# Optimization experiments

Hardware: AMD Instinct MI355X
Metric: run time of the kernel (lower is better)

Reference implementation:

```python
import jax, jax.numpy as jnp
import numpy as np

INPUTS = 512    # feature dim per timestep == seq len T == max_length (required by module math)
HIDDEN = 512
OUTPUTS = 512
MAXLEN = INPUTS
BATCH = 256


def setup_inputs() -> dict:
    key = jax.random.key(0)
    ks = jax.random.split(key, 7)
    def lin(k, out_f, in_f):
        bound = 1.0 / np.sqrt(in_f)
        return jax.random.uniform(k, (out_f, in_f), jnp.float32, -bound, bound)
    return {
        "x": jax.random.normal(ks[0], (BATCH, INPUTS * MAXLEN), jnp.float32),
        "W_attn": lin(ks[1], MAXLEN, HIDDEN + INPUTS),
        "b_attn": jnp.zeros((MAXLEN,), jnp.float32),
        "W_comb": lin(ks[2], HIDDEN, INPUTS + MAXLEN),
        "b_comb": jnp.zeros((HIDDEN,), jnp.float32),
        "W_ih": lin(ks[3], 3 * HIDDEN, HIDDEN),
        "W_hh": lin(ks[4], 3 * HIDDEN, HIDDEN),
        "b_ih": jnp.zeros((3 * HIDDEN,), jnp.float32),
        "b_hh": jnp.zeros((3 * HIDDEN,), jnp.float32),
        "W_out": lin(ks[5], OUTPUTS, HIDDEN),
        "b_out": jnp.zeros((OUTPUTS,), jnp.float32),
    }


def reference(x, W_attn, b_attn, W_comb, b_comb, W_ih, W_hh, b_ih, b_hh, W_out, b_out):
    B = x.shape[0]
    H = HIDDEN
    xv = x.reshape(B, INPUTS, MAXLEN)      # [B, inputs, T]
    xs = jnp.transpose(xv, (2, 0, 1))      # [T, B, inputs] for scan over time

    def step(h, x_t):
        # Bahdanau-style attention over the inputs axis (M == inputs)
        aw = jax.nn.softmax(jnp.concatenate([x_t, h], axis=1) @ W_attn.T + b_attn, axis=1)  # [B, M]
        ctx = jnp.einsum('bm,bmt->bt', aw, xv)                                              # [B, T]
        g = jax.nn.relu(jnp.concatenate([x_t, ctx], axis=1) @ W_comb.T + b_comb)            # [B, H]
        # PyTorch GRU cell, gate order (r, z, n)
        gi = g @ W_ih.T + b_ih
        gh = h @ W_hh.T + b_hh
        r = jax.nn.sigmoid(gi[:, :H] + gh[:, :H])
        z = jax.nn.sigmoid(gi[:, H:2 * H] + gh[:, H:2 * H])
        n = jnp.tanh(gi[:, 2 * H:] + r * gh[:, 2 * H:])
        h_new = (1.0 - z) * n + z * h
        return h_new, None

    h0 = jnp.zeros((B, H), x.dtype)
    hT, _ = jax.lax.scan(step, h0, xs)
    return hT @ W_out.T + b_out  # [B, outputs]
```

## Files before the change

kernel.cpp:

```cpp
#include <hip/hip_runtime.h>

#define NB 256
#define NT 512
#define NI 512
#define NH 512
#define NG 1536
#define NBLK 512

typedef __attribute__((ext_vector_type(8))) short bf16x8;
typedef __attribute__((ext_vector_type(4))) float f32x4;
typedef __attribute__((ext_vector_type(2))) float f32x2;

#define MFMA(a, b, c) __builtin_amdgcn_mfma_f32_16x16x32_bf16((a), (b), (c), 0, 0, 0)

#define BAR_LEAF(g)   ((g) * 64)
#define BAR_ROOT      1024
#define BAR_GEN       1088
#define FLG_LOGIT(rt) (1152 + (rt) * 64)
#define FLG_GH(rt)    (1664 + (rt) * 64)
#define FLG_XT        1920
#define FLG_G(rg)     (2176 + (rg) * 64)
#define FLG_GP(b)     (2688 + (b) * 64)
#define BAR_WORDS     20480

__device__ __forceinline__ unsigned short f2bf(float f) {
  unsigned int u = __float_as_uint(f);
  u = u + 0x7FFFu + ((u >> 16) & 1u);
  return (unsigned short)(u >> 16);
}
__device__ __forceinline__ float bflo(unsigned int p) { return __uint_as_float(p << 16); }
__device__ __forceinline__ float bfhi(unsigned int p) { return __uint_as_float(p & 0xffff0000u); }
__device__ __forceinline__ float sigm(float x) { return 1.f / (1.f + __expf(-x)); }

__device__ __forceinline__ void stf(float* p, float v) {
  __hip_atomic_store(p, v, __ATOMIC_RELAXED, __HIP_MEMORY_SCOPE_AGENT);
}
__device__ __forceinline__ void stu32(void* p, unsigned v) {
  __hip_atomic_store((unsigned*)p, v, __ATOMIC_RELAXED, __HIP_MEMORY_SCOPE_AGENT);
}
__device__ __forceinline__ void stu64(void* p, unsigned long long v) {
  __hip_atomic_store((unsigned long long*)p, v, __ATOMIC_RELAXED, __HIP_MEMORY_SCOPE_AGENT);
}
__device__ __forceinline__ void ldg16(uint4& d, const void* p) {
  asm volatile("global_load_dwordx4 %0, %1, off sc1" : "=v"(d) : "v"(p));
}
__device__ __forceinline__ void ldg8(float2& d, const void* p) {
  asm volatile("global_load_dwordx2 %0, %1, off sc1" : "=v"(d) : "v"(p));
}
__device__ __forceinline__ void ldg4(float& d, const void* p) {
  asm volatile("global_load_dword %0, %1, off sc1" : "=v"(d) : "v"(p));
}
__device__ __forceinline__ void wait_vm0() {
  asm volatile("s_waitcnt vmcnt(0)" ::: "memory");
  __builtin_amdgcn_sched_barrier(0);
}
__device__ __forceinline__ bf16x8 as_frag(uint4 v) {
  union { uint4 u; bf16x8 f; } c; c.u = v; return c.f;
}

__device__ __forceinline__ void flag_add(unsigned* f) {
  __hip_atomic_fetch_add(f, 1u, __ATOMIC_RELAXED, __HIP_MEMORY_SCOPE_AGENT);
}
__device__ __forceinline__ void flag_wait(unsigned* f, unsigned target) {
  while (__hip_atomic_load(f, __ATOMIC_RELAXED, __HIP_MEMORY_SCOPE_AGENT) < target)
    __builtin_amdgcn_s_sleep(1);
}

__global__ __launch_bounds__(256) void cast_f32_bf16(const float* __restrict__ s,
                                                     unsigned short* __restrict__ d, int n) {
  int i = blockIdx.x * 256 + threadIdx.x;
  int stride = gridDim.x * 256;
  for (; i < n; i += stride) d[i] = f2bf(s[i]);
}

__global__ __launch_bounds__(256) void zt_fp8(unsigned short* __restrict__ XZ,
                                              float* __restrict__ Zsc,
                                              const unsigned short* __restrict__ Wc) {
  __shared__ unsigned short As[32][552];
  __shared__ float Zf[32][512];
  const int tid = threadIdx.x;
  const int row0 = blockIdx.x * 32;
  const uint4* src = (const uint4*)(XZ + (size_t)row0 * 512);
#pragma unroll
  for (int it = 0; it < 8; ++it) {
    int e8 = tid + it * 256;
    uint4 v = src[e8];
    *(uint4*)&As[e8 >> 6][(e8 & 63) * 8] = v;
  }
  __syncthreads();
  const int lane = tid & 63, w = tid >> 6;
  const int al = lane & 15, kg = lane >> 4;
  const int rbase = (w & 1) * 16;
  const int cbase = (w >> 1) * 256;
  for (int cc = 0; cc < 16; ++cc) {
    int col0 = cbase + cc * 16;
    f32x4 acc = {0.f, 0.f, 0.f, 0.f};
    const unsigned short* Bp = Wc + (size_t)(col0 + al) * 1024 + 512;
    for (int k = 0; k < 512; k += 32) {
      bf16x8 av = *(const bf16x8*)&As[rbase + al][k + kg * 8];
      bf16x8 bv = *(const bf16x8*)(Bp + k + kg * 8);
      acc = MFMA(av, bv, acc);
    }
#pragma unroll
    for (int r = 0; r < 4; ++r)
      Zf[rbase + kg * 4 + r][col0 + al] = acc[r];
  }
  __syncthreads();
  unsigned char* Z8 = (unsigned char*)XZ;
#pragma unroll 2
  for (int r8 = 0; r8 < 8; ++r8) {
    int row = w * 8 + r8;
    const float* vr = &Zf[row][lane * 8];
    float v0 = vr[0], v1 = vr[1], v2 = vr[2], v3 = vr[3];
    float v4 = vr[4], v5 = vr[5], v6 = vr[6], v7 = vr[7];
    float amax = fmaxf(fmaxf(fmaxf(fabsf(v0), fabsf(v1)), fmaxf(fabsf(v2), fabsf(v3))),
                       fmaxf(fmaxf(fabsf(v4), fabsf(v5)), fmaxf(fabsf(v6), fabsf(v7))));
#pragma unroll
    for (int off = 32; off >= 1; off >>= 1) amax = fmaxf(amax, __shfl_xor(amax, off));
    float inv = amax > 0.f ? 448.f / amax : 0.f;
    int w0 = __builtin_amdgcn_cvt_pk_fp8_f32(v0 * inv, v1 * inv, 0, false);
    w0 = __builtin_amdgcn_cvt_pk_fp8_f32(v2 * inv, v3 * inv, w0, true);
    int w1 = __builtin_amdgcn_cvt_pk_fp8_f32(v4 * inv, v5 * inv, 0, false);
    w1 = __builtin_amdgcn_cvt_pk_fp8_f32(v6 * inv, v7 * inv, w1, true);
    uint2 o; o.x = (unsigned)w0; o.y = (unsigned)w1;
    *(uint2*)(Z8 + ((size_t)(row0 + row) << 10) + lane * 8) = o;
    if (lane == 0) Zsc[row0 + row] = amax * (1.f / 448.f);
  }
}

__global__ __launch_bounds__(256) void init_kernel(const float* __restrict__ x,
                                                   unsigned short* __restrict__ Xt,
                                                   unsigned short* __restrict__ Hbf,
                                                   unsigned* __restrict__ bar) {
  int idx = blockIdx.x * 256 + threadIdx.x;
  if (idx < BAR_WORDS) bar[idx] = 0u;
  if (idx < NB * NI) {
    int b = idx >> 9, i = idx & 511;
    Xt[idx] = f2bf(x[((size_t)b * 512 + i) * 512]);
    Hbf[idx] = 0;
  }
}

__global__ __launch_bounds__(256) void lxgx0_kernel(const unsigned short* __restrict__ Xt0,
                                                    const unsigned short* __restrict__ Wa,
                                                    const unsigned short* __restrict__ Wc,
                                                    const float* __restrict__ b_comb,
                                                    float* __restrict__ Lx,
                                                    float* __restrict__ Gx) {
  const int tid = threadIdx.x, lane = tid & 63, w = tid >> 6;
  const int al = lane & 15, kg = lane >> 4;
  int T = blockIdx.x;
  int m = T >> 7, tt = T & 127;
  int rt = tt >> 4, ct = tt & 15;
  int row0 = rt * 32 + (w & 1) * 16, col0 = ct * 32 + (w >> 1) * 16;
  const unsigned short* A = Xt0 + (size_t)(row0 + al) * NI;
  const unsigned short* B = (m ? Wc : Wa) + (size_t)(col0 + al) * 1024;
  f32x4 acc = {0.f, 0.f, 0.f, 0.f};
  for (int k = 0; k < 512; k += 32)
    acc = MFMA(*(const bf16x8*)(A + k + kg * 8), *(const bf16x8*)(B + k + kg * 8), acc);
  float* dst = m ? Gx : Lx;
  float bias = m ? b_comb[col0 + al] : 0.f;
#pragma unroll
  for (int r = 0; r < 4; ++r) {
    int row = row0 + kg * 4 + r;
    dst[row * NI + col0 + al] = acc[r] + bias;
  }
}

struct KParams {
  const unsigned char* Z8;
  const float* Zsc;
  const unsigned short* Wa;
  const unsigned short* Whh;
  const unsigned short* Wc;
  const unsigned short* Wih;
  const unsigned short* Wout;
  unsigned short* Xt;
  unsigned short* Hbf;
  unsigned short* Gbf;
  float* logits;
  float* gh;
  float* Lx;
  float* Gx;
  float* Gp;
  const float* x;
  const float* b_attn;
  const float* b_hh;
  const float* b_ih;
  const float* b_comb;
  const float* b_out;
  float* out;
  unsigned* bar;
};

__device__ __forceinline__ void gbar(unsigned* bar, unsigned gen_expect) {
  asm volatile("s_waitcnt vmcnt(0)" ::: "memory");
  __syncthreads();
  if (threadIdx.x == 0) {
    unsigned old = __hip_atomic_fetch_add(&bar[BAR_LEAF(blockIdx.x >> 5)], 1u,
                                          __ATOMIC_RELAXED, __HIP_MEMORY_SCOPE_AGENT);
    if ((old & 31) == 31) {
      unsigned ro = __hip_atomic_fetch_add(&bar[BAR_ROOT], 1u,
                                           __ATOMIC_RELAXED, __HIP_MEMORY_SCOPE_AGENT);
      if ((ro & 15) == 15)
        __hip_atomic_fetch_add(&bar[BAR_GEN], 1u,
                               __ATOMIC_RELAXED, __HIP_MEMORY_SCOPE_AGENT);
    }
    while (__hip_atomic_load(&bar[BAR_GEN], __ATOMIC_RELAXED, __HIP_MEMORY_SCOPE_AGENT) < gen_expect)
      __builtin_amdgcn_s_sleep(2);
    asm volatile("" ::: "memory");
  }
  __syncthreads();
}

__global__ __launch_bounds__(256, 2) void persistent_kernel(KParams P) {
  __shared__ float aw[512];
  __shared__ float4 pA[4][64];
  __shared__ float4 pB[4][64];
  __shared__ float red[8];
  const int bid = blockIdx.x, tid = threadIdx.x;
  const int lane = tid & 63, w = tid >> 6;
  const int al = lane & 15, kg = lane >> 4;

  f32x4 hreg = {0.f, 0.f, 0.f, 0.f};

  for (int t = 0; t < NT; ++t) {
    const int p = t & 1, np = p ^ 1;
    if (bid < 128) {
      int rt = bid >> 4, ct = bid & 15;
      int row0 = rt * 32 + (w & 1) * 16, col0 = ct * 32 + (w >> 1) * 16;
      const unsigned short* Ah = P.Hbf + (size_t)(row0 + al) * NH;
      const unsigned short* B = P.Wa + (size_t)(col0 + al) * 1024 + 512;
      uint4 fh[16];
      float lx[4];
#pragma unroll
      for (int i = 0; i < 16; ++i) ldg16(fh[i], Ah + i * 32 + kg * 8);
      {
        const float* lxp = P.Lx + (size_t)p * (NB * NI) + (size_t)(row0 + kg * 4) * NI + col0 + al;
#pragma unroll
        for (int r = 0; r < 4; ++r) ldg4(lx[r], lxp + (size_t)r * NI);
      }
      wait_vm0();
      f32x4 a1 = {0.f, 0.f, 0.f, 0.f};
#pragma unroll
      for (int i = 0; i < 16; ++i)
        a1 = MFMA(as_frag(fh[i]), *(const bf16x8*)(B + i * 32 + kg * 8), a1);
#pragma unroll
      for (int r = 0; r < 4; ++r) {
        int row = row0 + kg * 4 + r;
        stf(&P.logits[row * NI + col0 + al], lx[r] + a1[r] + P.b_attn[col0 + al]);
      }
      __syncthreads();
      if (tid == 0) flag_add(&P.bar[FLG_LOGIT(rt)]);
    } else if (bid < 320) {
      int bb = bid - 128;
      int rt = bb / 48, ct = bb % 48;
      int row0 = rt * 64 + w * 16, col0 = ct * 32;
      const unsigned short* Ah = P.Hbf + (size_t)(row0 + al) * NH;
      const unsigned short* B0 = P.Whh + (size_t)(col0 + al) * 512;
      const unsigned short* B1 = P.Whh + (size_t)(col0 + 16 + al) * 512;
      uint4 fa[16];
#pragma unroll
      for (int i = 0; i < 16; ++i) ldg16(fa[i], Ah + i * 32 + kg * 8);
      wait_vm0();
      f32x4 a0 = {0.f, 0.f, 0.f, 0.f}, a1 = {0.f, 0.f, 0.f, 0.f};
#pragma unroll
      for (int i = 0; i < 16; ++i) {
        a0 = MFMA(as_frag(fa[i]), *(const bf16x8*)(B0 + i * 32 + kg * 8), a0);
        a1 = MFMA(as_frag(fa[i]), *(const bf16x8*)(B1 + i * 32 + kg * 8), a1);
      }
#pragma unroll
      for (int r = 0; r < 4; ++r) {
        int row = row0 + kg * 4 + r;
        stf(&P.gh[row * NG + col0 + al], a0[r] + P.b_hh[col0 + al]);
        stf(&P.gh[row * NG + col0 + 16 + al], a1[r] + P.b_hh[col0 + 16 + al]);
      }
      __syncthreads();
      if (tid == 0) flag_add(&P.bar[FLG_GH(rt)]);
    } else if (bid < 384) {
    } else {
      if (t < NT - 1) {
        for (int e2 = (bid - 384) * 256 + tid; e2 < NB * NI / 2; e2 += 128 * 256) {
          int b = e2 >> 8, i = (e2 & 255) * 2;
          const float* xp = P.x + ((size_t)b * 512 + i) * 512 + t + 1;
          unsigned lo = f2bf(xp[0]);
          unsigned hi = f2bf(xp[512]);
          stu32(&P.Xt[(size_t)np * (NB * NI) + b * 512 + i], lo | (hi << 16));
        }
        __syncthreads();
        if (tid == 0) flag_add(&P.bar[FLG_XT]);
      }
    }

    {
      const int b = bid >> 1, mh = bid & 1;
      if (tid == 0) flag_wait(&P.bar[FLG_LOGIT(b >> 5)], 16u * (t + 1));
      __syncthreads();
      float2 lv;
      ldg8(lv, P.logits + (size_t)b * NI + 2 * tid);
      wait_vm0();
      float mx = fmaxf(lv.x, lv.y);
#pragma unroll
      for (int off = 32; off >= 1; off >>= 1) mx = fmaxf(mx, __shfl_xor(mx, off));
      if (lane == 0) red[w] = mx;
      __syncthreads();
      mx = fmaxf(fmaxf(red[0], red[1]), fmaxf(red[2], red[3]));
      float e0 = __expf(lv.x - mx), e1 = __expf(lv.y - mx);
      float sm = e0 + e1;
#pragma unroll
      for (int off = 32; off >= 1; off >>= 1) sm += __shfl_xor(sm, off);
      if (lane == 0) red[4 + w] = sm;
      __syncthreads();
      sm = (red[4] + red[5]) + (red[6] + red[7]);
      float inv = 1.f / sm;
      float2 scl = *(const float2*)(P.Zsc + (size_t)b * 512 + 2 * tid);
      aw[2 * tid] = e0 * inv * scl.x;
      aw[2 * tid + 1] = e1 * inv * scl.y;
      __syncthreads();

      const unsigned char* Zb = P.Z8 + (((size_t)b * 512 + mh * 256 + w * 64) << 10) + lane * 8;
      const float* awp = aw + mh * 256 + w * 64;
      float c0 = 0.f, c1 = 0.f, c2 = 0.f, c3 = 0.f, c4 = 0.f, c5 = 0.f, c6 = 0.f, c7 = 0.f;
#pragma unroll
      for (int mm = 0; mm < 64; mm += 16) {
        uint2 px[16];
#pragma unroll
        for (int u = 0; u < 16; ++u) px[u] = *(const uint2*)(Zb + ((size_t)(mm + u) << 10));
#pragma unroll
        for (int u = 0; u < 16; ++u) {
          float a_ = awp[mm + u];
          f32x2 d0 = __builtin_amdgcn_cvt_pk_f32_fp8((int)px[u].x, false);
          f32x2 d1 = __builtin_amdgcn_cvt_pk_f32_fp8((int)px[u].x, true);
          f32x2 d2 = __builtin_amdgcn_cvt_pk_f32_fp8((int)px[u].y, false);
          f32x2 d3 = __builtin_amdgcn_cvt_pk_f32_fp8((int)px[u].y, true);
          c0 = fmaf(a_, d0[0], c0); c1 = fmaf(a_, d0[1], c1);
          c2 = fmaf(a_, d1[0], c2); c3 = fmaf(a_, d1[1], c3);
          c4 = fmaf(a_, d2[0], c4); c5 = fmaf(a_, d2[1], c5);
          c6 = fmaf(a_, d3[0], c6); c7 = fmaf(a_, d3[1], c7);
        }
      }
      pA[w][lane] = make_float4(c0, c1, c2, c3);
      pB[w][lane] = make_float4(c4, c5, c6, c7);
      __syncthreads();
      float s0_, s1_, s2_, s3_, s4_, s5_, s6_, s7_;
      if (w == 0) {
        float4 a0_ = pA[0][lane], a1_ = pA[1][lane], a2_ = pA[2][lane], a3_ = pA[3][lane];
        float4 b0_ = pB[0][lane], b1_ = pB[1][lane], b2_ = pB[2][lane], b3_ = pB[3][lane];
        s0_ = (a0_.x + a1_.x) + (a2_.x + a3_.x);
        s1_ = (a0_.y + a1_.y) + (a2_.y + a3_.y);
        s2_ = (a0_.z + a1_.z) + (a2_.z + a3_.z);
        s3_ = (a0_.w + a1_.w) + (a2_.w + a3_.w);
        s4_ = (b0_.x + b1_.x) + (b2_.x + b3_.x);
        s5_ = (b0_.y + b1_.y) + (b2_.y + b3_.y);
        s6_ = (b0_.z + b1_.z) + (b2_.z + b3_.z);
        s7_ = (b0_.w + b1_.w) + (b2_.w + b3_.w);
      }
      if (mh == 0) {
        if (w == 0) {
          float* gp = P.Gp + (size_t)b * NH + lane * 8;
          union { float f[2]; unsigned long long q; } q0, q1, q2, q3;
          q0.f[0] = s0_; q0.f[1] = s1_;
          q1.f[0] = s2_; q1.f[1] = s3_;
          q2.f[0] = s4_; q2.f[1] = s5_;
          q3.f[0] = s6_; q3.f[1] = s7_;
          stu64(gp, q0.q); stu64(gp + 2, q1.q); stu64(gp + 4, q2.q); stu64(gp + 6, q3.q);
        }
        __syncthreads();
        if (tid == 0) flag_add(&P.bar[FLG_GP(b)]);
      } else {
        __syncthreads();
        if (tid == 0) flag_wait(&P.bar[FLG_GP(b)], (unsigned)(t + 1));
        __syncthreads();
        if (w == 0) {
          const float* gp = P.Gp + (size_t)b * NH + lane * 8;
          const float* gxp = P.Gx + (size_t)p * (NB * NH) + (size_t)b * NH + lane * 8;
          float2 r0, r1, r2, r3, x0, x1, x2, x3;
          ldg8(r0, gp);     ldg8(r1, gp + 2);
          ldg8(r2, gp + 4); ldg8(r3, gp + 6);
          ldg8(x0, gxp);     ldg8(x1, gxp + 2);
          ldg8(x2, gxp + 4); ldg8(x3, gxp + 6);
          wait_vm0();
          float v0 = fmaxf(x0.x + r0.x + s0_, 0.f);
          float v1 = fmaxf(x0.y + r0.y + s1_, 0.f);
          float v2 = fmaxf(x1.x + r1.x + s2_, 0.f);
          float v3 = fmaxf(x1.y + r1.y + s3_, 0.f);
          float v4 = fmaxf(x2.x + r2.x + s4_, 0.f);
          float v5 = fmaxf(x2.y + r2.y + s5_, 0.f);
          float v6 = fmaxf(x3.x + r3.x + s6_, 0.f);
          float v7 = fmaxf(x3.y + r3.y + s7_, 0.f);
          unsigned long long o0 =
              (unsigned long long)((unsigned)f2bf(v0) | ((unsigned)f2bf(v1) << 16)) |
              ((unsigned long long)((unsigned)f2bf(v2) | ((unsigned)f2bf(v3) << 16)) << 32);
          unsigned long long o1 =
              (unsigned long long)((unsigned)f2bf(v4) | ((unsigned)f2bf(v5) << 16)) |
              ((unsigned long long)((unsigned)f2bf(v6) | ((unsigned)f2bf(v7) << 16)) << 32);
          stu64(P.Gbf + (size_t)b * NH + lane * 8, o0);
          stu64(P.Gbf + (size_t)b * NH + lane * 8 + 4, o1);
        }
        __syncthreads();
        if (tid == 0) flag_add(&P.bar[FLG_G(b >> 5)]);
      }
    }

    if (bid >= 384) {
      int q = bid - 384;
      int rt = q >> 4, ct = q & 15;
      int row0 = rt * 32 + (w & 1) * 16;
      int j0 = ct * 32 + (w >> 1) * 16;
      if (tid == 0) {
        flag_wait(&P.bar[FLG_G(rt)], 32u * (t + 1));
        flag_wait(&P.bar[FLG_GH(rt >> 1)], 48u * (t + 1));
      }
      __syncthreads();
      const unsigned short* Ag = P.Gbf + (size_t)(row0 + al) * NH;
      const unsigned short* Br = P.Wih + (size_t)(j0 + al) * 512;
      const unsigned short* Bz = P.Wih + (size_t)(j0 + 512 + al) * 512;
      const unsigned short* Bn = P.Wih + (size_t)(j0 + 1024 + al) * 512;
      int j = j0 + al;
      uint4 fa[16];
      float ghv[4][3];
#pragma unroll
      for (int i = 0; i < 16; ++i) ldg16(fa[i], Ag + i * 32 + kg * 8);
#pragma unroll
      for (int r = 0; r < 4; ++r) {
        const float* ghrow = P.gh + (size_t)(row0 + kg * 4 + r) * NG + j;
        ldg4(ghv[r][0], ghrow);
        ldg4(ghv[r][1], ghrow + 512);
        ldg4(ghv[r][2], ghrow + 1024);
      }
      wait_vm0();
      f32x4 ar = {0.f, 0.f, 0.f, 0.f}, az = {0.f, 0.f, 0.f, 0.f}, an = {0.f, 0.f, 0.f, 0.f};
#pragma unroll
      for (int i = 0; i < 16; ++i) {
        ar = MFMA(as_frag(fa[i]), *(const bf16x8*)(Br + i * 32 + kg * 8), ar);
        az = MFMA(as_frag(fa[i]), *(const bf16x8*)(Bz + i * 32 + kg * 8), az);
        an = MFMA(as_frag(fa[i]), *(const bf16x8*)(Bn + i * 32 + kg * 8), an);
      }
      float bir = P.b_ih[j], biz = P.b_ih[j + 512], bin_ = P.b_ih[j + 1024];
#pragma unroll
      for (int r = 0; r < 4; ++r) {
        int row = row0 + kg * 4 + r;
        float rg = sigm(ar[r] + bir + ghv[r][0]);
        float zg = sigm(az[r] + biz + ghv[r][1]);
        float ng = tanhf(an[r] + bin_ + rg * ghv[r][2]);
        float hn = (1.f - zg) * ng + zg * hreg[r];
        hreg[r] = hn;
        unsigned hv = f2bf(hn);
        unsigned ov = __shfl_xor((int)hv, 1);
        if ((al & 1) == 0)
          stu32(&P.Hbf[(size_t)row * NH + (j & ~1)], hv | (ov << 16));
      }
    } else if (bid >= 320) {
      if (t < NT - 1) {
        if (tid == 0) flag_wait(&P.bar[FLG_XT], 128u * (t + 1));
        __syncthreads();
        int q = bid - 320;
        for (int jj = 0; jj < 4; ++jj) {
          int T = q + 64 * jj;
          int m = T >> 7, tt = T & 127;
          int rt = tt >> 4, ct = tt & 15;
          int row0 = rt * 32 + (w & 1) * 16, col0 = ct * 32 + (w >> 1) * 16;
          const unsigned short* A = P.Xt + (size_t)np * (NB * NI) + (size_t)(row0 + al) * NI;
          const unsigned short* B = (m ? P.Wc : P.Wa) + (size_t)(col0 + al) * 1024;
          uint4 fa[16];
#pragma unroll
          for (int i = 0; i < 16; ++i) ldg16(fa[i], A + i * 32 + kg * 8);
          wait_vm0();
          f32x4 acc = {0.f, 0.f, 0.f, 0.f};
#pragma unroll
          for (int i = 0; i < 16; ++i)
            acc = MFMA(as_frag(fa[i]), *(const bf16x8*)(B + i * 32 + kg * 8), acc);
          float* dst = (m ? P.Gx : P.Lx) + (size_t)np * (NB * NI);
          float bias = m ? P.b_comb[col0 + al] : 0.f;
#pragma unroll
          for (int r = 0; r < 4; ++r) {
            int row = row0 + kg * 4 + r;
            stf(&dst[row * NI + col0 + al], acc[r] + bias);
          }
        }
      }
    }
    gbar(P.bar, (unsigned)(t + 1));
  }

  if (bid < 128) {
    int rt = bid >> 4, ct = bid & 15;
    int row0 = rt * 32 + (w & 1) * 16;
    int col0 = ct * 32 + (w >> 1) * 16;
    const unsigned short* Ah = P.Hbf + (size_t)(row0 + al) * NH;
    const unsigned short* B0 = P.Wout + (size_t)(col0 + al) * 512;
    uint4 fa[16];
#pragma unroll
    for (int i = 0; i < 16; ++i) ldg16(fa[i], Ah + i * 32 + kg * 8);
    wait_vm0();
    f32x4 acc = {0.f, 0.f, 0.f, 0.f};
#pragma unroll
    for (int i = 0; i < 16; ++i) acc = MFMA(as_frag(fa[i]), *(const bf16x8*)(B0 + i * 32 + kg * 8), acc);
#pragma unroll
    for (int r = 0; r < 4; ++r) {
      int row = row0 + kg * 4 + r;
      P.out[row * 512 + col0 + al] = acc[r] + P.b_out[col0 + al];
    }
  }
}

extern "C" void kernel_launch(void* const* d_in, const int* in_sizes, int n_in,
                              void* d_out, int out_size, void* d_ws, size_t ws_size,
                              hipStream_t stream) {
  const float* x      = (const float*)d_in[0];
  const float* W_attn = (const float*)d_in[1];
  const float* b_attn = (const float*)d_in[2];
  const float* W_comb = (const float*)d_in[3];
  const float* b_comb = (const float*)d_in[4];
  const float* W_ih   = (const float*)d_in[5];
  const float* W_hh   = (const float*)d_in[6];
  const float* b_ih   = (const float*)d_in[7];
  const float* b_hh   = (const float*)d_in[8];
  const float* W_out  = (const float*)d_in[9];
  const float* b_out  = (const float*)d_in[10];

  char* wp = (char*)d_ws;
  size_t off = 0;
  unsigned short* XZ   = (unsigned short*)(wp + off); off += (size_t)NB * NI * NH * 2;
  unsigned short* Wa   = (unsigned short*)(wp + off); off += (size_t)NI * 1024 * 2;
  unsigned short* Whh  = (unsigned short*)(wp + off); off += (size_t)NG * 512 * 2;
  unsigned short* Wc   = (unsigned short*)(wp + off); off += (size_t)NH * 1024 * 2;
  unsigned short* Wih  = (unsigned short*)(wp + off); off += (size_t)NG * 512 * 2;
  unsigned short* Wout = (unsigned short*)(wp + off); off += (size_t)512 * 512 * 2;
  unsigned short* Xt   = (unsigned short*)(wp + off); off += (size_t)2 * NB * NI * 2;
  unsigned short* Hbf  = (unsigned short*)(wp + off); off += (size_t)NB * NH * 2;
  unsigned short* Gbf  = (unsigned short*)(wp + off); off += (size_t)NB * NH * 2;
  float* logits        = (float*)(wp + off); off += (size_t)NB * NI * 4;
  float* gh            = (float*)(wp + off); off += (size_t)NB * NG * 4;
  float* Lx            = (float*)(wp + off); off += (size_t)2 * NB * NI * 4;
  float* Gx            = (float*)(wp + off); off += (size_t)2 * NB * NI * 4;
  float* Gp            = (float*)(wp + off); off += (size_t)NB * NH * 4;
  float* Zsc           = (float*)(wp + off); off += (size_t)NB * NI * 4;
  unsigned* bar        = (unsigned*)(wp + off); off += (size_t)BAR_WORDS * 4 + 4096;

  cast_f32_bf16<<<8192, 256, 0, stream>>>(x, XZ, NB * NI * NT);
  cast_f32_bf16<<<512, 256, 0, stream>>>(W_attn, Wa, NI * 1024);
  cast_f32_bf16<<<512, 256, 0, stream>>>(W_hh, Whh, NG * 512);
  cast_f32_bf16<<<512, 256, 0, stream>>>(W_comb, Wc, NH * 1024);
  cast_f32_bf16<<<512, 256, 0, stream>>>(W_ih, Wih, NG * 512);
  cast_f32_bf16<<<512, 256, 0, stream>>>(W_out, Wout, 512 * 512);
  zt_fp8<<<4096, 256, 0, stream>>>(XZ, Zsc, Wc);
  init_kernel<<<512, 256, 0, stream>>>(x, Xt, Hbf, bar);
  lxgx0_kernel<<<256, 256, 0, stream>>>(Xt, Wa, Wc, b_comb, Lx, Gx);

  KParams prm;
  prm.Z8 = (const unsigned char*)XZ; prm.Zsc = Zsc;
  prm.Wa = Wa; prm.Whh = Whh; prm.Wc = Wc; prm.Wih = Wih; prm.Wout = Wout;
  prm.Xt = Xt; prm.Hbf = Hbf; prm.Gbf = Gbf;
  prm.logits = logits; prm.gh = gh; prm.Lx = Lx; prm.Gx = Gx; prm.Gp = Gp;
  prm.x = x; prm.b_attn = b_attn; prm.b_hh = b_hh; prm.b_ih = b_ih; prm.b_out = b_out;
  prm.b_comb = b_comb;
  prm.out = (float*)d_out;
  prm.bar = bar;

  void* kargs[] = { &prm };
  hipError_t e = hipLaunchCooperativeKernel((const void*)persistent_kernel,
                                            dim3(NBLK), dim3(256), kargs, 0, stream);
  if (e != hipSuccess) {
    persistent_kernel<<<dim3(NBLK), dim3(256), 0, stream>>>(prm);
  }
}
```

Measured before the change: 31.96 ms.

## Retile FP8 Z storage into 32-row blocks for 16-byte context loads

The precomputed FP8 Z matrix is now stored per producer block in contiguous 32-row by 512-byte tiles, not as full 1024-byte rows. The context reduction reads 16 bytes per lane across two half-waves, cutting the number of load instructions. A cross-half shuffle and shared-memory transpose then spread the final reduction over all threads instead of one wave. This raises register use and requires the Z layout and indexing to stay consistent between producer and consumer.

```diff
diff --git a/kernel.cpp b/kernel.cpp
--- a/kernel.cpp
+++ b/kernel.cpp
@@ -106,7 +106,7 @@
       Zf[rbase + kg * 4 + r][col0 + al] = acc[r];
   }
   __syncthreads();
-  unsigned char* Z8 = (unsigned char*)XZ;
+  unsigned char* Z8 = (unsigned char*)XZ + ((size_t)blockIdx.x << 15);
 #pragma unroll 2
   for (int r8 = 0; r8 < 8; ++r8) {
     int row = w * 8 + r8;
@@ -123,7 +123,7 @@
     int w1 = __builtin_amdgcn_cvt_pk_fp8_f32(v4 * inv, v5 * inv, 0, false);
     w1 = __builtin_amdgcn_cvt_pk_fp8_f32(v6 * inv, v7 * inv, w1, true);
     uint2 o; o.x = (unsigned)w0; o.y = (unsigned)w1;
-    *(uint2*)(Z8 + ((size_t)(row0 + row) << 10) + lane * 8) = o;
+    *(uint2*)(Z8 + ((size_t)row << 9) + lane * 8) = o;
     if (lane == 0) Zsc[row0 + row] = amax * (1.f / 448.f);
   }
 }
@@ -215,8 +215,7 @@
 
 __global__ __launch_bounds__(256, 2) void persistent_kernel(KParams P) {
   __shared__ float aw[512];
-  __shared__ float4 pA[4][64];
-  __shared__ float4 pB[4][64];
+  __shared__ float pS[4][32][16];
   __shared__ float red[8];
   const int bid = blockIdx.x, tid = threadIdx.x;
   const int lane = tid & 63, w = tid >> 6;
@@ -318,85 +317,69 @@
       aw[2 * tid + 1] = e1 * inv * scl.y;
       __syncthreads();
 
-      const unsigned char* Zb = P.Z8 + (((size_t)b * 512 + mh * 256 + w * 64) << 10) + lane * 8;
+      const int half = lane >> 5, hl = lane & 31;
+      const unsigned char* Zb = P.Z8 + ((size_t)(b * 16 + mh * 8 + w * 2) << 15)
+                               + (size_t)hl * 16 + (size_t)half * 512;
       const float* awp = aw + mh * 256 + w * 64;
-      float c0 = 0.f, c1 = 0.f, c2 = 0.f, c3 = 0.f, c4 = 0.f, c5 = 0.f, c6 = 0.f, c7 = 0.f;
-#pragma unroll
-      for (int mm = 0; mm < 64; mm += 16) {
-        uint2 px[16];
-#pragma unroll
-        for (int u = 0; u < 16; ++u) px[u] = *(const uint2*)(Zb + ((size_t)(mm + u) << 10));
-#pragma unroll
-        for (int u = 0; u < 16; ++u) {
-          float a_ = awp[mm + u];
-          f32x2 d0 = __builtin_amdgcn_cvt_pk_f32_fp8((int)px[u].x, false);
-          f32x2 d1 = __builtin_amdgcn_cvt_pk_f32_fp8((int)px[u].x, true);
-          f32x2 d2 = __builtin_amdgcn_cvt_pk_f32_fp8((int)px[u].y, false);
-          f32x2 d3 = __builtin_amdgcn_cvt_pk_f32_fp8((int)px[u].y, true);
-          c0 = fmaf(a_, d0[0], c0); c1 = fmaf(a_, d0[1], c1);
-          c2 = fmaf(a_, d1[0], c2); c3 = fmaf(a_, d1[1], c3);
-          c4 = fmaf(a_, d2[0], c4); c5 = fmaf(a_, d2[1], c5);
-          c6 = fmaf(a_, d3[0], c6); c7 = fmaf(a_, d3[1], c7);
+      float acc[16];
+#pragma unroll
+      for (int i = 0; i < 16; ++i) acc[i] = 0.f;
+#pragma unroll
+      for (int gg = 0; gg < 2; ++gg) {
+        uint4 px[16];
+#pragma unroll
+        for (int k = 0; k < 16; ++k)
+          px[k] = *(const uint4*)(Zb + ((size_t)gg << 15) + ((size_t)k << 10));
+#pragma unroll
+        for (int k = 0; k < 16; ++k) {
+          float a_ = awp[gg * 32 + 2 * k + half];
+          f32x2 d0 = __builtin_amdgcn_cvt_pk_f32_fp8((int)px[k].x, false);
+          f32x2 d1 = __builtin_amdgcn_cvt_pk_f32_fp8((int)px[k].x, true);
+          f32x2 d2 = __builtin_amdgcn_cvt_pk_f32_fp8((int)px[k].y, false);
+          f32x2 d3 = __builtin_amdgcn_cvt_pk_f32_fp8((int)px[k].y, true);
+          f32x2 d4 = __builtin_amdgcn_cvt_pk_f32_fp8((int)px[k].z, false);
+          f32x2 d5 = __builtin_amdgcn_cvt_pk_f32_fp8((int)px[k].z, true);
+          f32x2 d6 = __builtin_amdgcn_cvt_pk_f32_fp8((int)px[k].w, false);
+          f32x2 d7 = __builtin_amdgcn_cvt_pk_f32_fp8((int)px[k].w, true);
+          acc[0]  = fmaf(a_, d0[0], acc[0]);  acc[1]  = fmaf(a_, d0[1], acc[1]);
+          acc[2]  = fmaf(a_, d1[0], acc[2]);  acc[3]  = fmaf(a_, d1[1], acc[3]);
+          acc[4]  = fmaf(a_, d2[0], acc[4]);  acc[5]  = fmaf(a_, d2[1], acc[5]);
+          acc[6]  = fmaf(a_, d3[0], acc[6]);  acc[7]  = fmaf(a_, d3[1], acc[7]);
+          acc[8]  = fmaf(a_, d4[0], acc[8]);  acc[9]  = fmaf(a_, d4[1], acc[9]);
+          acc[10] = fmaf(a_, d5[0], acc[10]); acc[11] = fmaf(a_, d5[1], acc[11]);
+          acc[12] = fmaf(a_, d6[0], acc[12]); acc[13] = fmaf(a_, d6[1], acc[13]);
+          acc[14] = fmaf(a_, d7[0], acc[14]); acc[15] = fmaf(a_, d7[1], acc[15]);
         }
       }
-      pA[w][lane] = make_float4(c0, c1, c2, c3);
-      pB[w][lane] = make_float4(c4, c5, c6, c7);
-      __syncthreads();
-      float s0_, s1_, s2_, s3_, s4_, s5_, s6_, s7_;
-      if (w == 0) {
-        float4 a0_ = pA[0][lane], a1_ = pA[1][lane], a2_ = pA[2][lane], a3_ = pA[3][lane];
-        float4 b0_ = pB[0][lane], b1_ = pB[1][lane], b2_ = pB[2][lane], b3_ = pB[3][lane];
-        s0_ = (a0_.x + a1_.x) + (a2_.x + a3_.x);
-        s1_ = (a0_.y + a1_.y) + (a2_.y + a3_.y);
-        s2_ = (a0_.z + a1_.z) + (a2_.z + a3_.z);
-        s3_ = (a0_.w + a1_.w) + (a2_.w + a3_.w);
-        s4_ = (b0_.x + b1_.x) + (b2_.x + b3_.x);
-        s5_ = (b0_.y + b1_.y) + (b2_.y + b3_.y);
-        s6_ = (b0_.z + b1_.z) + (b2_.z + b3_.z);
-        s7_ = (b0_.w + b1_.w) + (b2_.w + b3_.w);
-      }
+#pragma unroll
+      for (int i = 0; i < 16; ++i) acc[i] += __shfl_xor(acc[i], 32);
+      if (lane < 32) {
+#pragma unroll
+        for (int i = 0; i < 16; ++i) pS[w][hl][i] = acc[i];
+      }
+      __syncthreads();
+      const int c0 = 2 * tid, c1 = 2 * tid + 1;
+      float s0 = (pS[0][c0 >> 4][c0 & 15] + pS[1][c0 >> 4][c0 & 15])
+               + (pS[2][c0 >> 4][c0 & 15] + pS[3][c0 >> 4][c0 & 15]);
+      float s1 = (pS[0][c1 >> 4][c1 & 15] + pS[1][c1 >> 4][c1 & 15])
+               + (pS[2][c1 >> 4][c1 & 15] + pS[3][c1 >> 4][c1 & 15]);
       if (mh == 0) {
-        if (w == 0) {
-          float* gp = P.Gp + (size_t)b * NH + lane * 8;
-          union { float f[2]; unsigned long long q; } q0, q1, q2, q3;
-          q0.f[0] = s0_; q0.f[1] = s1_;
-          q1.f[0] = s2_; q1.f[1] = s3_;
-          q2.f[0] = s4_; q2.f[1] = s5_;
-          q3.f[0] = s6_; q3.f[1] = s7_;
-          stu64(gp, q0.q); stu64(gp + 2, q1.q); stu64(gp + 4, q2.q); stu64(gp + 6, q3.q);
-        }
+        union { float f[2]; unsigned long long q; } q0;
+        q0.f[0] = s0; q0.f[1] = s1;
+        stu64(&P.Gp[(size_t)b * NH + c0], q0.q);
         __syncthreads();
         if (tid == 0) flag_add(&P.bar[FLG_GP(b)]);
       } else {
         __syncthreads();
         if (tid == 0) flag_wait(&P.bar[FLG_GP(b)], (unsigned)(t + 1));
         __syncthreads();
-        if (w == 0) {
-          const float* gp = P.Gp + (size_t)b * NH + lane * 8;
-          const float* gxp = P.Gx + (size_t)p * (NB * NH) + (size_t)b * NH + lane * 8;
-          float2 r0, r1, r2, r3, x0, x1, x2, x3;
-          ldg8(r0, gp);     ldg8(r1, gp + 2);
-          ldg8(r2, gp + 4); ldg8(r3, gp + 6);
-          ldg8(x0, gxp);     ldg8(x1, gxp + 2);
-          ldg8(x2, gxp + 4); ldg8(x3, gxp + 6);
-          wait_vm0();
-          float v0 = fmaxf(x0.x + r0.x + s0_, 0.f);
-          float v1 = fmaxf(x0.y + r0.y + s1_, 0.f);
-          float v2 = fmaxf(x1.x + r1.x + s2_, 0.f);
-          float v3 = fmaxf(x1.y + r1.y + s3_, 0.f);
-          float v4 = fmaxf(x2.x + r2.x + s4_, 0.f);
-          float v5 = fmaxf(x2.y + r2.y + s5_, 0.f);
-          float v6 = fmaxf(x3.x + r3.x + s6_, 0.f);
-          float v7 = fmaxf(x3.y + r3.y + s7_, 0.f);
-          unsigned long long o0 =
-              (unsigned long long)((unsigned)f2bf(v0) | ((unsigned)f2bf(v1) << 16)) |
-              ((unsigned long long)((unsigned)f2bf(v2) | ((unsigned)f2bf(v3) << 16)) << 32);
-          unsigned long long o1 =
-              (unsigned long long)((unsigned)f2bf(v4) | ((unsigned)f2bf(v5) << 16)) |
-              ((unsigned long long)((unsigned)f2bf(v6) | ((unsigned)f2bf(v7) << 16)) << 32);
-          stu64(P.Gbf + (size_t)b * NH + lane * 8, o0);
-          stu64(P.Gbf + (size_t)b * NH + lane * 8 + 4, o1);
-        }
+        float2 gp2, gx2;
+        ldg8(gp2, &P.Gp[(size_t)b * NH + c0]);
+        ldg8(gx2, P.Gx + (size_t)p * (NB * NH) + (size_t)b * NH + c0);
+        wait_vm0();
+        float v0 = fmaxf(gx2.x + gp2.x + s0, 0.f);
+        float v1 = fmaxf(gx2.y + gp2.y + s1, 0.f);
+        stu32(&P.Gbf[(size_t)b * NH + c0], (unsigned)f2bf(v0) | ((unsigned)f2bf(v1) << 16));
         __syncthreads();
         if (tid == 0) flag_add(&P.bar[FLG_G(b >> 5)]);
       }
```

New measurement: 30.44 ms. 1.05x faster.
